# Performance work log

Measured on AMD Instinct MI355X. Metric: run time of the kernel, lower is better.

The kernel has to match this reference:

```python
import jax, jax.numpy as jnp
import numpy as np

N_NODES = 50000
N_EDGES = 150000
N_GRAPHS = 1024
IN_DIM = 78
OUT_DIM = 64
HEADS = 10
HID = OUT_DIM * HEADS  # 640
NEG_SLOPE = 0.2


def _add_self_loops(edge_index, num_nodes):
    loop = jnp.arange(num_nodes, dtype=edge_index.dtype)
    src = jnp.concatenate([edge_index[0], loop])
    dst = jnp.concatenate([edge_index[1], loop])
    return src, dst


def gatv2_conv(x, edge_index, Wl, Wr, att, bias, heads, out_dim):
    # PyG GATv2Conv (share_weights=False, concat=True, add_self_loops=True),
    # inference mode so attention dropout is a no-op.
    N = x.shape[0]
    src, dst = _add_self_loops(edge_index, N)
    xl = (x @ Wl).reshape(N, heads, out_dim)  # source transform
    xr = (x @ Wr).reshape(N, heads, out_dim)  # target transform
    s = jax.nn.leaky_relu(xl[src] + xr[dst], NEG_SLOPE)      # [E,H,C]
    logits = jnp.einsum('ehc,hc->eh', s, att)                # [E,H]
    m = jax.ops.segment_max(logits, dst, num_segments=N)     # [N,H] (self-loops => no empty segs)
    ex = jnp.exp(logits - m[dst])
    den = jax.ops.segment_sum(ex, dst, num_segments=N)
    alpha = ex / den[dst]                                    # scatter-softmax over in-edges
    out = jax.ops.segment_sum(alpha[:, :, None] * xl[src], dst, num_segments=N)
    return out.reshape(N, heads * out_dim) + bias


def gcn_conv(x, edge_index, W, b):
    N = x.shape[0]
    src, dst = _add_self_loops(edge_index, N)
    deg = jax.ops.segment_sum(jnp.ones(src.shape[0], x.dtype), dst, num_segments=N)
    dinv = jax.lax.rsqrt(jnp.maximum(deg, 1.0))
    norm = dinv[src] * dinv[dst]                             # [E]
    xw = x @ W
    return jax.ops.segment_sum(norm[:, None] * xw[src], dst, num_segments=N) + b


def setup_inputs() -> dict:
    key = jax.random.key(0)
    ks = jax.random.split(key, 16)
    x = jax.random.normal(ks[0], (N_NODES, IN_DIM), dtype=jnp.float32)
    edge_index = jax.random.randint(ks[1], (2, N_EDGES), 0, N_NODES, dtype=jnp.int64)
    batch = jnp.sort(jax.random.randint(ks[2], (N_NODES,), 0, N_GRAPHS, dtype=jnp.int64))

    def glorot(k, shape, fan_in):
        return jax.random.normal(k, shape, dtype=jnp.float32) * (1.0 / np.sqrt(fan_in))

    return {
        'x': x, 'edge_index': edge_index, 'batch': batch,
        'Wl1': glorot(ks[3], (IN_DIM, HID), IN_DIM),
        'Wr1': glorot(ks[4], (IN_DIM, HID), IN_DIM),
        'a1': glorot(ks[5], (HEADS, OUT_DIM), OUT_DIM),
        'b1': jnp.zeros((HID,), jnp.float32),
        'Wl2': glorot(ks[6], (HID, HID), HID),
        'Wr2': glorot(ks[7], (HID, HID), HID),
        'a2': glorot(ks[8], (1, HID), HID),
        'b2': jnp.zeros((HID,), jnp.float32),
        'Wg': glorot(ks[9], (HID, HID), HID),
        'bg': jnp.zeros((HID,), jnp.float32),
    }


def reference(x, edge_index, batch, Wl1, Wr1, a1, b1, Wl2, Wr2, a2, b2, Wg, bg):
    # inference: feature dropout layers are identity
    h = jax.nn.elu(gatv2_conv(x, edge_index, Wl1, Wr1, a1, b1, HEADS, OUT_DIM))
    h = gatv2_conv(h, edge_index, Wl2, Wr2, a2, b2, 1, HID)
    h = gcn_conv(h, edge_index, Wg, bg)
    h = jax.nn.relu(h)
    # global max pool + global mean pool per graph
    gmax = jax.ops.segment_max(h, batch, num_segments=N_GRAPHS)
    cnt = jax.ops.segment_sum(jnp.ones((h.shape[0],), h.dtype), batch, num_segments=N_GRAPHS)
    gmean = jax.ops.segment_sum(h, batch, num_segments=N_GRAPHS) / jnp.maximum(cnt, 1.0)[:, None]
    return jnp.concatenate([gmax, gmean], axis=1)
```

## Files before the change

### kernel.cpp

```cpp
#include <hip/hip_runtime.h>
#include <hip/hip_bf16.h>
#include <cstdint>
#include <cstddef>

typedef __hip_bfloat16 bf16;

#define N_NODES  50000
#define N_EDGES  150000
#define N_GRAPHS 1024
#define IN_DIM   78
#define K1P      128
#define OUT_DIM  64
#define HEADS    10
#define HID      640
#define NEG_SLOPE 0.2f
#define SCB      ((N_NODES + 255) / 256)

static __device__ __forceinline__ float b2f(bf16 v){ return __bfloat162float(v); }
static __device__ __forceinline__ bf16  f2b(float v){ return __float2bfloat16(v); }

__device__ __forceinline__ int clampi(int v, int hi){ return v < 0 ? 0 : (v >= hi ? hi - 1 : v); }

__device__ __forceinline__ float bf2f_bits(short s){
  return __uint_as_float(((unsigned)(unsigned short)s) << 16);
}
__device__ __forceinline__ short f2bf_bits(float v){
  unsigned u = __float_as_uint(v);
  return (short)((u + 0x7fffu + ((u >> 16) & 1u)) >> 16);
}

__global__ __launch_bounds__(256) void fill_u32(unsigned* __restrict__ p, unsigned v, int n){
  int i = blockIdx.x * 256 + threadIdx.x;
  if (i < n) p[i] = v;
}

__global__ __launch_bounds__(256) void conv_x(const float* __restrict__ x, bf16* __restrict__ XB){
  int i = blockIdx.x * 256 + threadIdx.x;
  if (i >= N_NODES * K1P) return;
  int n = i / K1P, k = i - n * K1P;
  XB[i] = f2b(k < IN_DIM ? x[(size_t)n * IN_DIM + k] : 0.f);
}

__global__ __launch_bounds__(256) void conv_wT2(const float* __restrict__ W0,
                                                const float* __restrict__ W1,
                                                bf16* __restrict__ WT,
                                                int K, int N, int Kp){
  int i = blockIdx.x * 256 + threadIdx.x;
  const int per = N * Kp;
  if (i >= 2 * per) return;
  int m = i / per, r = i - m * per;
  const float* W = m == 0 ? W0 : W1;
  int n = r / Kp, k = r - n * Kp;
  WT[i] = f2b(k < K ? W[(size_t)k * N + n] : 0.f);
}

__global__ __launch_bounds__(256) void conv_wT3t(const float* __restrict__ W0,
                                                 const float* __restrict__ W1,
                                                 const float* __restrict__ W2,
                                                 bf16* __restrict__ WT){
  __shared__ float t[32][33];
  int m = blockIdx.z;
  const float* W = m == 0 ? W0 : (m == 1 ? W1 : W2);
  int n0 = blockIdx.x * 32, k0 = blockIdx.y * 32;
  int tx = threadIdx.x & 31, ty = threadIdx.x >> 5;
#pragma unroll
  for (int r = 0; r < 32; r += 8)
    t[ty + r][tx] = W[(size_t)(k0 + ty + r) * HID + n0 + tx];
  __syncthreads();
  bf16* O = WT + (size_t)m * HID * HID;
#pragma unroll
  for (int r = 0; r < 32; r += 8)
    O[(size_t)(n0 + ty + r) * HID + k0 + tx] = f2b(t[tx][ty + r]);
}

#define BM 128
#define BN 128
#define BK 64

typedef __attribute__((ext_vector_type(8))) short bf16x8;
typedef __attribute__((ext_vector_type(4))) float f32x4;

typedef const __attribute__((address_space(1))) unsigned gu32;
typedef __attribute__((address_space(3))) unsigned lu32;

__global__ __launch_bounds__(256) void mfma_gemm(const bf16* __restrict__ A,
                                                 const bf16* __restrict__ BT,
                                                 bf16* __restrict__ C0,
                                                 bf16* __restrict__ C1,
                                                 int M, int Kp, int NB){
  int d   = blockIdx.x;
  int xcd = d & 7, j = d >> 3;
  int cb  = j % NB, ri = j / NB;
  int rb  = ri * 8 + xcd;
  const int row0 = rb * BM;
  if (row0 >= M) return;
  const int col0 = cb * BN;

  __shared__ short As[BM * BK];
  __shared__ short Bs[BN * BK];
  const int tid  = threadIdx.x;
  const int lane = tid & 63;
  const int wave = tid >> 6;
  const int wr   = (wave >> 1) * 64;
  const int wc   = (wave & 1) * 64;
  const int l15  = lane & 15;
  const int quad = lane >> 4;
  const int sw   = l15 & 7;

  const bf16* aptr[4];
  const bf16* bptr[4];
  lu32* lda[4];
  lu32* ldb[4];
#pragma unroll
  for (int t = 0; t < 4; ++t){
    int ci = (t * 4 + wave) * 64 + lane;
    int r  = ci >> 3;
    int sc = (ci & 7) ^ (r & 7);
    int gr = row0 + r; if (gr >= M) gr = M - 1;
    aptr[t] = A  + (size_t)gr * Kp + sc * 8;
    bptr[t] = BT + (size_t)(col0 + r) * Kp + sc * 8;
    lda[t]  = (lu32*)(&As[(t * 4 + wave) * 512]);
    ldb[t]  = (lu32*)(&Bs[(t * 4 + wave) * 512]);
  }

  f32x4 acc[4][4];
#pragma unroll
  for (int i = 0; i < 4; ++i)
#pragma unroll
    for (int jj = 0; jj < 4; ++jj) acc[i][jj] = (f32x4){0.f, 0.f, 0.f, 0.f};

  for (int k0 = 0; k0 < Kp; k0 += BK){
#pragma unroll
    for (int t = 0; t < 4; ++t){
      __builtin_amdgcn_global_load_lds((gu32*)(aptr[t] + k0), lda[t], 16, 0, 0);
      __builtin_amdgcn_global_load_lds((gu32*)(bptr[t] + k0), ldb[t], 16, 0, 0);
    }
    __syncthreads();

#pragma unroll
    for (int ks = 0; ks < 2; ++ks){
      const int slotA = ((ks * 4 + quad) ^ sw) * 8;
      bf16x8 af[4], bfr[4];
#pragma unroll
      for (int i = 0; i < 4; ++i)
        af[i] = *(bf16x8*)(&As[(wr + i * 16 + l15) * BK + slotA]);
#pragma unroll
      for (int jj = 0; jj < 4; ++jj)
        bfr[jj] = *(bf16x8*)(&Bs[(wc + jj * 16 + l15) * BK + slotA]);
#pragma unroll
      for (int i = 0; i < 4; ++i)
#pragma unroll
        for (int jj = 0; jj < 4; ++jj)
          acc[i][jj] = __builtin_amdgcn_mfma_f32_16x16x32_bf16(af[i], bfr[jj], acc[i][jj], 0, 0, 0);
    }
    __syncthreads();
  }

  if (row0 + BM <= M){
#pragma unroll
    for (int i = 0; i < 4; ++i){
#pragma unroll
      for (int jj = 0; jj < 4; ++jj){
        int gc = col0 + wc + jj * 16 + l15;
        bf16* Cp = (gc < HID) ? C0 : C1;
        size_t cc = (gc < HID) ? gc : gc - HID;
        size_t base = (size_t)(row0 + wr + i * 16 + quad * 4) * HID + cc;
#pragma unroll
        for (int r = 0; r < 4; ++r)
          Cp[base + (size_t)r * HID] = f2b(acc[i][jj][r]);
      }
    }
  } else {
#pragma unroll
    for (int i = 0; i < 4; ++i){
#pragma unroll
      for (int jj = 0; jj < 4; ++jj){
        int gc = col0 + wc + jj * 16 + l15;
        bf16* Cp = (gc < HID) ? C0 : C1;
        int cc   = (gc < HID) ? gc : gc - HID;
#pragma unroll
        for (int r = 0; r < 4; ++r){
          int gr = row0 + wr + i * 16 + quad * 4 + r;
          if (gr < M) Cp[(size_t)gr * HID + cc] = f2b(acc[i][jj][r]);
        }
      }
    }
  }
}

__global__ __launch_bounds__(256) void count_deg(const int* __restrict__ edst, int* __restrict__ degi){
  int e = blockIdx.x * 256 + threadIdx.x;
  if (e >= N_EDGES) return;
  atomicAdd(&degi[clampi(edst[e], N_NODES)], 1);
}

__global__ __launch_bounds__(256) void scan_blk(const int* __restrict__ degi,
                                                int* __restrict__ rowp,
                                                float* __restrict__ dinv,
                                                int* __restrict__ bsum){
  __shared__ int wsum[4];
  int b = blockIdx.x, tid = threadIdx.x;
  int i = b * 256 + tid;
  int lane = tid & 63, wv = tid >> 6;
  int v = (i < N_NODES) ? degi[i] : 0;
  int incl = v;
#pragma unroll
  for (int ofs = 1; ofs < 64; ofs <<= 1){
    int t = __shfl_up(incl, ofs);
    if (lane >= ofs) incl += t;
  }
  if (lane == 63) wsum[wv] = incl;
  __syncthreads();
  int woff = 0;
#pragma unroll
  for (int w = 0; w < 4; ++w) if (w < wv) woff += wsum[w];
  if (i < N_NODES){
    rowp[i] = woff + incl - v;
    dinv[i] = rsqrtf((float)(v + 1));
  }
  if (tid == 0) bsum[b] = wsum[0] + wsum[1] + wsum[2] + wsum[3];
}

__global__ __launch_bounds__(256) void scan_top(int* __restrict__ bsum, int* __restrict__ rowp){
  __shared__ int wsum[4];
  int tid = threadIdx.x, lane = tid & 63, wv = tid >> 6;
  int v = (tid < SCB) ? bsum[tid] : 0;
  int incl = v;
#pragma unroll
  for (int ofs = 1; ofs < 64; ofs <<= 1){
    int t = __shfl_up(incl, ofs);
    if (lane >= ofs) incl += t;
  }
  if (lane == 63) wsum[wv] = incl;
  __syncthreads();
  int woff = 0;
#pragma unroll
  for (int w = 0; w < 4; ++w) if (w < wv) woff += wsum[w];
  if (tid < SCB) bsum[tid] = woff + incl - v;
  if (tid == 255) rowp[N_NODES] = woff + incl;
}

__global__ __launch_bounds__(256) void scan_add(const int* __restrict__ bsum,
                                                int* __restrict__ rowp,
                                                int* __restrict__ curs){
  int i = blockIdx.x * 256 + threadIdx.x;
  if (i >= N_NODES) return;
  int r = rowp[i] + bsum[blockIdx.x];
  rowp[i] = r; curs[i] = r;
}

__global__ __launch_bounds__(256) void bucket_edges(const int* __restrict__ esrc,
                                                    const int* __restrict__ edst,
                                                    int* __restrict__ curs,
                                                    int* __restrict__ srcg,
                                                    int* __restrict__ dstg){
  int e = blockIdx.x * 256 + threadIdx.x;
  if (e >= N_EDGES) return;
  int d = clampi(edst[e], N_NODES);
  int pos = atomicAdd(&curs[d], 1);
  srcg[pos] = clampi(esrc[e], N_NODES);
  dstg[pos] = d;
}

__global__ __launch_bounds__(256) void gat1_fused(const bf16* __restrict__ xl,
                                                  const bf16* __restrict__ xr,
                                                  const int* __restrict__ srcg,
                                                  const int* __restrict__ rowp,
                                                  const float* __restrict__ att,
                                                  const float* __restrict__ bias,
                                                  bf16* __restrict__ H){
  int n    = (blockIdx.x * 256 + threadIdx.x) >> 6;
  int lane = threadIdx.x & 63;
  if (n >= N_NODES) return;
  int r0 = rowp[n], r1 = rowp[n + 1];

  float4 aA0 = *(const float4*)(att + 8 * lane);
  float4 aA1 = *(const float4*)(att + 8 * lane + 4);
  float2 aBv = *(const float2*)(att + 512 + 2 * lane);
  float attA[8] = {aA0.x, aA0.y, aA0.z, aA0.w, aA1.x, aA1.y, aA1.z, aA1.w};
  float attB0 = aBv.x, attB1 = aBv.y;

  const bf16* xrn = xr + (size_t)n * HID;
  bf16x8 vr = *(const bf16x8*)(xrn + 8 * lane);
  unsigned ur = *(const unsigned*)(xrn + 512 + 2 * lane);
  float xrA[8];
#pragma unroll
  for (int j = 0; j < 8; ++j) xrA[j] = bf2f_bits(vr[j]);
  float xrB0 = bf2f_bits((short)(ur & 0xffff));
  float xrB1 = bf2f_bits((short)(ur >> 16));

  auto logits = [&](const float* xA, float xB0, float xB1, float& lA, float& lB){
    float pa = 0.f;
#pragma unroll
    for (int j = 0; j < 8; ++j){
      float s = xA[j] + xrA[j];
      s *= (s > 0.f) ? 1.f : NEG_SLOPE;
      pa = fmaf(attA[j], s, pa);
    }
    pa += __shfl_xor(pa, 1);
    pa += __shfl_xor(pa, 2);
    pa += __shfl_xor(pa, 4);
    lA = pa;
    float s0 = xB0 + xrB0; s0 *= (s0 > 0.f) ? 1.f : NEG_SLOPE;
    float s1 = xB1 + xrB1; s1 *= (s1 > 0.f) ? 1.f : NEG_SLOPE;
    float pb = attB0 * s0 + attB1 * s1;
    pb += __shfl_xor(pb, 1);
    pb += __shfl_xor(pb, 2);
    pb += __shfl_xor(pb, 4);
    pb += __shfl_xor(pb, 8);
    pb += __shfl_xor(pb, 16);
    lB = pb;
  };

  float accA[8], accB0, accB1, lsA, lsB;
  float denA = 1.f, denB = 1.f;

  {
    const bf16* xn = xl + (size_t)n * HID;
    bf16x8 v0 = *(const bf16x8*)(xn + 8 * lane);
    unsigned u0 = *(const unsigned*)(xn + 512 + 2 * lane);
    float sA[8];
#pragma unroll
    for (int j = 0; j < 8; ++j){ sA[j] = bf2f_bits(v0[j]); accA[j] = sA[j]; }
    float sB0 = bf2f_bits((short)(u0 & 0xffff));
    float sB1 = bf2f_bits((short)(u0 >> 16));
    accB0 = sB0; accB1 = sB1;
    logits(sA, sB0, sB1, lsA, lsB);
  }

  auto upd1 = [&](const float* yA, float yB0, float yB1){
    float lA, lB;
    logits(yA, yB0, yB1, lA, lB);
    float pA = __expf(fminf(lA - lsA, 60.f));
    float pB = __expf(fminf(lB - lsB, 60.f));
    denA += pA; denB += pB;
#pragma unroll
    for (int j = 0; j < 8; ++j) accA[j] = fmaf(pA, yA[j], accA[j]);
    accB0 = fmaf(pB, yB0, accB0);
    accB1 = fmaf(pB, yB1, accB1);
  };

  int p = r0;
  for (; p + 3 < r1; p += 4){
    int s0i = srcg[p], s1i = srcg[p + 1], s2i = srcg[p + 2], s3i = srcg[p + 3];
    const bf16* q0 = xl + (size_t)s0i * HID;
    const bf16* q1 = xl + (size_t)s1i * HID;
    const bf16* q2 = xl + (size_t)s2i * HID;
    const bf16* q3 = xl + (size_t)s3i * HID;
    bf16x8 w0 = *(const bf16x8*)(q0 + 8 * lane);
    bf16x8 w1 = *(const bf16x8*)(q1 + 8 * lane);
    bf16x8 w2 = *(const bf16x8*)(q2 + 8 * lane);
    bf16x8 w3 = *(const bf16x8*)(q3 + 8 * lane);
    unsigned t0 = *(const unsigned*)(q0 + 512 + 2 * lane);
    unsigned t1 = *(const unsigned*)(q1 + 512 + 2 * lane);
    unsigned t2 = *(const unsigned*)(q2 + 512 + 2 * lane);
    unsigned t3 = *(const unsigned*)(q3 + 512 + 2 * lane);
    {
      float yA0[8];
#pragma unroll
      for (int j = 0; j < 8; ++j) yA0[j] = bf2f_bits(w0[j]);
      upd1(yA0, bf2f_bits((short)(t0 & 0xffff)), bf2f_bits((short)(t0 >> 16)));
    }
    {
      float yA1[8];
#pragma unroll
      for (int j = 0; j < 8; ++j) yA1[j] = bf2f_bits(w1[j]);
      upd1(yA1, bf2f_bits((short)(t1 & 0xffff)), bf2f_bits((short)(t1 >> 16)));
    }
    {
      float yA2[8];
#pragma unroll
      for (int j = 0; j < 8; ++j) yA2[j] = bf2f_bits(w2[j]);
      upd1(yA2, bf2f_bits((short)(t2 & 0xffff)), bf2f_bits((short)(t2 >> 16)));
    }
    {
      float yA3[8];
#pragma unroll
      for (int j = 0; j < 8; ++j) yA3[j] = bf2f_bits(w3[j]);
      upd1(yA3, bf2f_bits((short)(t3 & 0xffff)), bf2f_bits((short)(t3 >> 16)));
    }
  }
  for (; p < r1; ++p){
    int si = srcg[p];
    const bf16* q0 = xl + (size_t)si * HID;
    bf16x8 w0 = *(const bf16x8*)(q0 + 8 * lane);
    unsigned t0 = *(const unsigned*)(q0 + 512 + 2 * lane);
    float yA0[8];
#pragma unroll
    for (int j = 0; j < 8; ++j) yA0[j] = bf2f_bits(w0[j]);
    upd1(yA0, bf2f_bits((short)(t0 & 0xffff)), bf2f_bits((short)(t0 >> 16)));
  }

  float invA = 1.f / denA, invB = 1.f / denB;
  float4 bA0 = *(const float4*)(bias + 8 * lane);
  float4 bA1 = *(const float4*)(bias + 8 * lane + 4);
  float2 bB  = *(const float2*)(bias + 512 + 2 * lane);
  float bAa[8] = {bA0.x, bA0.y, bA0.z, bA0.w, bA1.x, bA1.y, bA1.z, bA1.w};
  bf16x8 oA;
#pragma unroll
  for (int j = 0; j < 8; ++j){
    float v = accA[j] * invA + bAa[j];
    v = v > 0.f ? v : (__expf(v) - 1.f);
    oA[j] = f2bf_bits(v);
  }
  float vb0 = accB0 * invB + bB.x; vb0 = vb0 > 0.f ? vb0 : (__expf(vb0) - 1.f);
  float vb1 = accB1 * invB + bB.y; vb1 = vb1 > 0.f ? vb1 : (__expf(vb1) - 1.f);
  bf16* hn = H + (size_t)n * HID;
  *(bf16x8*)(hn + 8 * lane) = oA;
  unsigned ob = (unsigned)(unsigned short)f2bf_bits(vb0) |
                ((unsigned)(unsigned short)f2bf_bits(vb1) << 16);
  *(unsigned*)(hn + 512 + 2 * lane) = ob;
}

__global__ __launch_bounds__(256) void gat2_fused(const bf16* __restrict__ xl,
                                                  const bf16* __restrict__ xr,
                                                  const int* __restrict__ srcg,
                                                  const int* __restrict__ rowp,
                                                  const float* __restrict__ att,
                                                  const float* __restrict__ bias,
                                                  bf16* __restrict__ H){
  int n    = (blockIdx.x * 256 + threadIdx.x) >> 6;
  int lane = threadIdx.x & 63;
  if (n >= N_NODES) return;
  int r0 = rowp[n], r1 = rowp[n + 1];

  float4 aA0 = *(const float4*)(att + 8 * lane);
  float4 aA1 = *(const float4*)(att + 8 * lane + 4);
  float2 aBv = *(const float2*)(att + 512 + 2 * lane);
  float attA[8] = {aA0.x, aA0.y, aA0.z, aA0.w, aA1.x, aA1.y, aA1.z, aA1.w};
  float attB0 = aBv.x, attB1 = aBv.y;

  const bf16* xrn = xr + (size_t)n * HID;
  bf16x8 vr = *(const bf16x8*)(xrn + 8 * lane);
  unsigned ur = *(const unsigned*)(xrn + 512 + 2 * lane);
  float xrA[8];
#pragma unroll
  for (int j = 0; j < 8; ++j) xrA[j] = bf2f_bits(vr[j]);
  float xrB0 = bf2f_bits((short)(ur & 0xffff));
  float xrB1 = bf2f_bits((short)(ur >> 16));

  auto logit1 = [&](const float* xA, float xB0, float xB1)->float{
    float s0 = xB0 + xrB0; s0 *= (s0 > 0.f) ? 1.f : NEG_SLOPE;
    float s1 = xB1 + xrB1; s1 *= (s1 > 0.f) ? 1.f : NEG_SLOPE;
    float pa = attB0 * s0 + attB1 * s1;
#pragma unroll
    for (int j = 0; j < 8; ++j){
      float s = xA[j] + xrA[j];
      s *= (s > 0.f) ? 1.f : NEG_SLOPE;
      pa = fmaf(attA[j], s, pa);
    }
    pa += __shfl_xor(pa, 1);
    pa += __shfl_xor(pa, 2);
    pa += __shfl_xor(pa, 4);
    pa += __shfl_xor(pa, 8);
    pa += __shfl_xor(pa, 16);
    pa += __shfl_xor(pa, 32);
    return pa;
  };

  float accA[8], accB0, accB1, ls;
  float den = 1.f;
  {
    const bf16* xn = xl + (size_t)n * HID;
    bf16x8 v0 = *(const bf16x8*)(xn + 8 * lane);
    unsigned u0 = *(const unsigned*)(xn + 512 + 2 * lane);
    float sA[8];
#pragma unroll
    for (int j = 0; j < 8; ++j){ sA[j] = bf2f_bits(v0[j]); accA[j] = sA[j]; }
    float sB0 = bf2f_bits((short)(u0 & 0xffff));
    float sB1 = bf2f_bits((short)(u0 >> 16));
    accB0 = sB0; accB1 = sB1;
    ls = logit1(sA, sB0, sB1);
  }

  auto upd1 = [&](const float* yA, float yB0, float yB1){
    float l = logit1(yA, yB0, yB1);
    float pv = __expf(fminf(l - ls, 60.f));
    den += pv;
#pragma unroll
    for (int j = 0; j < 8; ++j) accA[j] = fmaf(pv, yA[j], accA[j]);
    accB0 = fmaf(pv, yB0, accB0);
    accB1 = fmaf(pv, yB1, accB1);
  };

  int p = r0;
  for (; p + 3 < r1; p += 4){
    int s0i = srcg[p], s1i = srcg[p + 1], s2i = srcg[p + 2], s3i = srcg[p + 3];
    const bf16* q0 = xl + (size_t)s0i * HID;
    const bf16* q1 = xl + (size_t)s1i * HID;
    const bf16* q2 = xl + (size_t)s2i * HID;
    const bf16* q3 = xl + (size_t)s3i * HID;
    bf16x8 w0 = *(const bf16x8*)(q0 + 8 * lane);
    bf16x8 w1 = *(const bf16x8*)(q1 + 8 * lane);
    bf16x8 w2 = *(const bf16x8*)(q2 + 8 * lane);
    bf16x8 w3 = *(const bf16x8*)(q3 + 8 * lane);
    unsigned t0 = *(const unsigned*)(q0 + 512 + 2 * lane);
    unsigned t1 = *(const unsigned*)(q1 + 512 + 2 * lane);
    unsigned t2 = *(const unsigned*)(q2 + 512 + 2 * lane);
    unsigned t3 = *(const unsigned*)(q3 + 512 + 2 * lane);
    {
      float yA0[8];
#pragma unroll
      for (int j = 0; j < 8; ++j) yA0[j] = bf2f_bits(w0[j]);
      upd1(yA0, bf2f_bits((short)(t0 & 0xffff)), bf2f_bits((short)(t0 >> 16)));
    }
    {
      float yA1[8];
#pragma unroll
      for (int j = 0; j < 8; ++j) yA1[j] = bf2f_bits(w1[j]);
      upd1(yA1, bf2f_bits((short)(t1 & 0xffff)), bf2f_bits((short)(t1 >> 16)));
    }
    {
      float yA2[8];
#pragma unroll
      for (int j = 0; j < 8; ++j) yA2[j] = bf2f_bits(w2[j]);
      upd1(yA2, bf2f_bits((short)(t2 & 0xffff)), bf2f_bits((short)(t2 >> 16)));
    }
    {
      float yA3[8];
#pragma unroll
      for (int j = 0; j < 8; ++j) yA3[j] = bf2f_bits(w3[j]);
      upd1(yA3, bf2f_bits((short)(t3 & 0xffff)), bf2f_bits((short)(t3 >> 16)));
    }
  }
  for (; p < r1; ++p){
    int si = srcg[p];
    const bf16* q0 = xl + (size_t)si * HID;
    bf16x8 w0 = *(const bf16x8*)(q0 + 8 * lane);
    unsigned t0 = *(const unsigned*)(q0 + 512 + 2 * lane);
    float yA0[8];
#pragma unroll
    for (int j = 0; j < 8; ++j) yA0[j] = bf2f_bits(w0[j]);
    upd1(yA0, bf2f_bits((short)(t0 & 0xffff)), bf2f_bits((short)(t0 >> 16)));
  }

  float inv = 1.f / den;
  float4 bA0 = *(const float4*)(bias + 8 * lane);
  float4 bA1 = *(const float4*)(bias + 8 * lane + 4);
  float2 bB  = *(const float2*)(bias + 512 + 2 * lane);
  float bAa[8] = {bA0.x, bA0.y, bA0.z, bA0.w, bA1.x, bA1.y, bA1.z, bA1.w};
  bf16x8 oA;
#pragma unroll
  for (int j = 0; j < 8; ++j) oA[j] = f2bf_bits(accA[j] * inv + bAa[j]);
  bf16* hn = H + (size_t)n * HID;
  *(bf16x8*)(hn + 8 * lane) = oA;
  unsigned ob = (unsigned)(unsigned short)f2bf_bits(accB0 * inv + bB.x) |
                ((unsigned)(unsigned short)f2bf_bits(accB1 * inv + bB.y) << 16);
  *(unsigned*)(hn + 512 + 2 * lane) = ob;
}

__global__ __launch_bounds__(256) void gcn_gather(const bf16* __restrict__ xw,
                                                  const int* __restrict__ srcg,
                                                  const int* __restrict__ rowp,
                                                  const float* __restrict__ dinv,
                                                  const float* __restrict__ bg,
                                                  bf16* __restrict__ h3){
  int n    = (blockIdx.x * 256 + threadIdx.x) >> 6;
  int lane = threadIdx.x & 63;
  if (n >= N_NODES) return;
  int r0 = rowp[n], r1 = rowp[n + 1];

  float dn = dinv[n];
  float accA[8], accB[2];
  {
    float w = dn * dn;
    const bf16* xn = xw + (size_t)n * HID;
    bf16x8 va = *(const bf16x8*)(xn + 8 * lane);
    unsigned vb = *(const unsigned*)(xn + 512 + 2 * lane);
#pragma unroll
    for (int j = 0; j < 8; ++j) accA[j] = w * bf2f_bits(va[j]);
    accB[0] = w * bf2f_bits((short)(vb & 0xffff));
    accB[1] = w * bf2f_bits((short)(vb >> 16));
  }
  int p = r0;
  for (; p + 3 < r1; p += 4){
    int s0 = srcg[p], s1 = srcg[p + 1], s2 = srcg[p + 2], s3 = srcg[p + 3];
    const bf16* xs0 = xw + (size_t)s0 * HID;
    const bf16* xs1 = xw + (size_t)s1 * HID;
    const bf16* xs2 = xw + (size_t)s2 * HID;
    const bf16* xs3 = xw + (size_t)s3 * HID;
    float w0 = dinv[s0] * dn, w1 = dinv[s1] * dn, w2 = dinv[s2] * dn, w3 = dinv[s3] * dn;
    bf16x8 va0 = *(const bf16x8*)(xs0 + 8 * lane);
    bf16x8 va1 = *(const bf16x8*)(xs1 + 8 * lane);
    bf16x8 va2 = *(const bf16x8*)(xs2 + 8 * lane);
    bf16x8 va3 = *(const bf16x8*)(xs3 + 8 * lane);
    unsigned vb0 = *(const unsigned*)(xs0 + 512 + 2 * lane);
    unsigned vb1 = *(const unsigned*)(xs1 + 512 + 2 * lane);
    unsigned vb2 = *(const unsigned*)(xs2 + 512 + 2 * lane);
    unsigned vb3 = *(const unsigned*)(xs3 + 512 + 2 * lane);
#pragma unroll
    for (int j = 0; j < 8; ++j)
      accA[j] += w0 * bf2f_bits(va0[j]) + w1 * bf2f_bits(va1[j])
               + w2 * bf2f_bits(va2[j]) + w3 * bf2f_bits(va3[j]);
    accB[0] += w0 * bf2f_bits((short)(vb0 & 0xffff)) + w1 * bf2f_bits((short)(vb1 & 0xffff))
             + w2 * bf2f_bits((short)(vb2 & 0xffff)) + w3 * bf2f_bits((short)(vb3 & 0xffff));
    accB[1] += w0 * bf2f_bits((short)(vb0 >> 16))    + w1 * bf2f_bits((short)(vb1 >> 16))
             + w2 * bf2f_bits((short)(vb2 >> 16))    + w3 * bf2f_bits((short)(vb3 >> 16));
  }
  for (; p + 1 < r1; p += 2){
    int s0 = srcg[p], s1 = srcg[p + 1];
    float w0 = dinv[s0] * dn, w1 = dinv[s1] * dn;
    const bf16* xs0 = xw + (size_t)s0 * HID;
    const bf16* xs1 = xw + (size_t)s1 * HID;
    bf16x8 va0 = *(const bf16x8*)(xs0 + 8 * lane);
    bf16x8 va1 = *(const bf16x8*)(xs1 + 8 * lane);
    unsigned vb0 = *(const unsigned*)(xs0 + 512 + 2 * lane);
    unsigned vb1 = *(const unsigned*)(xs1 + 512 + 2 * lane);
#pragma unroll
    for (int j = 0; j < 8; ++j) accA[j] += w0 * bf2f_bits(va0[j]) + w1 * bf2f_bits(va1[j]);
    accB[0] += w0 * bf2f_bits((short)(vb0 & 0xffff)) + w1 * bf2f_bits((short)(vb1 & 0xffff));
    accB[1] += w0 * bf2f_bits((short)(vb0 >> 16))    + w1 * bf2f_bits((short)(vb1 >> 16));
  }
  if (p < r1){
    int s = srcg[p];
    float w = dinv[s] * dn;
    const bf16* xs = xw + (size_t)s * HID;
    bf16x8 va = *(const bf16x8*)(xs + 8 * lane);
    unsigned vb = *(const unsigned*)(xs + 512 + 2 * lane);
#pragma unroll
    for (int j = 0; j < 8; ++j) accA[j] += w * bf2f_bits(va[j]);
    accB[0] += w * bf2f_bits((short)(vb & 0xffff));
    accB[1] += w * bf2f_bits((short)(vb >> 16));
  }
  float4 bA0 = *(const float4*)(bg + 8 * lane);
  float4 bA1 = *(const float4*)(bg + 8 * lane + 4);
  float2 bB  = *(const float2*)(bg + 512 + 2 * lane);
  float bAa[8] = {bA0.x, bA0.y, bA0.z, bA0.w, bA1.x, bA1.y, bA1.z, bA1.w};
  bf16x8 oA;
#pragma unroll
  for (int j = 0; j < 8; ++j) oA[j] = f2bf_bits(fmaxf(accA[j] + bAa[j], 0.f));
  bf16* hn = h3 + (size_t)n * HID;
  *(bf16x8*)(hn + 8 * lane) = oA;
  unsigned ob = (unsigned)(unsigned short)f2bf_bits(fmaxf(accB[0] + bB.x, 0.f)) |
                ((unsigned)(unsigned short)f2bf_bits(fmaxf(accB[1] + bB.y, 0.f)) << 16);
  *(unsigned*)(hn + 512 + 2 * lane) = ob;
}

__global__ __launch_bounds__(256) void graph_bounds(const int* __restrict__ batch,
                                                    int* __restrict__ gstart){
  int n = blockIdx.x * 256 + threadIdx.x;
  if (n >= N_NODES) return;
  int b = clampi(batch[n], N_GRAPHS);
  if (n == 0){
    for (int g = 0; g <= b; ++g) gstart[g] = 0;
  } else {
    int bp = clampi(batch[n - 1], N_GRAPHS);
    for (int g = bp + 1; g <= b; ++g) gstart[g] = n;
  }
  if (n == N_NODES - 1){
    for (int g = b + 1; g <= N_GRAPHS; ++g) gstart[g] = N_NODES;
  }
}

__global__ __launch_bounds__(320) void pool_graph(const bf16* __restrict__ h3,
                                                  const int* __restrict__ gstart,
                                                  float* __restrict__ out){
  int g = blockIdx.x;
  int c2 = threadIdx.x;
  int n0 = gstart[g], n1 = gstart[g + 1];
  float mx0 = 0.f, mx1 = 0.f, sm0 = 0.f, sm1 = 0.f;
  for (int n = n0; n < n1; ++n){
    unsigned v = *(const unsigned*)(h3 + (size_t)n * HID + 2 * c2);
    float a = bf2f_bits((short)(v & 0xffff));
    float b = bf2f_bits((short)(v >> 16));
    mx0 = fmaxf(mx0, a); sm0 += a;
    mx1 = fmaxf(mx1, b); sm1 += b;
  }
  float inv = (n1 > n0) ? 1.f / (float)(n1 - n0) : 0.f;
  float* og = out + (size_t)g * 2 * HID;
  og[2 * c2]             = mx0;
  og[2 * c2 + 1]         = mx1;
  og[HID + 2 * c2]       = sm0 * inv;
  og[HID + 2 * c2 + 1]   = sm1 * inv;
}

extern "C" void kernel_launch(void* const* d_in, const int* in_sizes, int n_in,
                              void* d_out, int out_size, void* d_ws, size_t ws_size,
                              hipStream_t stream){
  const float* x     = (const float*)d_in[0];
  const int*   ei    = (const int*)d_in[1];
  const int*   batch = (const int*)d_in[2];
  const float* Wl1 = (const float*)d_in[3];
  const float* Wr1 = (const float*)d_in[4];
  const float* a1  = (const float*)d_in[5];
  const float* b1  = (const float*)d_in[6];
  const float* Wl2 = (const float*)d_in[7];
  const float* Wr2 = (const float*)d_in[8];
  const float* a2  = (const float*)d_in[9];
  const float* b2  = (const float*)d_in[10];
  const float* Wg  = (const float*)d_in[11];
  const float* bg  = (const float*)d_in[12];
  const int* esrc = ei;
  const int* edst = ei + N_EDGES;

  char* ws = (char*)d_ws;
  size_t off = 0;
  auto take = [&](size_t bytes)->char*{
    char* p = ws + off; off = (off + bytes + 255) & ~(size_t)255; return p;
  };
  bf16*     X1   = (bf16*)    take((size_t)N_NODES * HID * 2);
  bf16*     X2   = (bf16*)    take((size_t)N_NODES * HID * 2);
  bf16*     H    = (bf16*)    take((size_t)N_NODES * HID * 2);
  bf16*     XB   = (bf16*)    take((size_t)N_NODES * K1P * 2);
  bf16*     WT1l = (bf16*)    take((size_t)HID * K1P * 2);
  bf16*     WT1r = (bf16*)    take((size_t)HID * K1P * 2);
  bf16*     WT2l = (bf16*)    take((size_t)HID * HID * 2);
  bf16*     WT2r = (bf16*)    take((size_t)HID * HID * 2);
  bf16*     WTg  = (bf16*)    take((size_t)HID * HID * 2);
  int*      DEGI = (int*)     take((size_t)N_NODES * 4);
  int*      ROWP = (int*)     take((size_t)(N_NODES + 1) * 4);
  int*      CURS = (int*)     take((size_t)N_NODES * 4);
  int*      SRCG = (int*)     take((size_t)N_EDGES * 4);
  int*      DSTG = (int*)     take((size_t)N_EDGES * 4);
  float*    DINV = (float*)   take((size_t)N_NODES * 4);
  int*      GST  = (int*)     take((size_t)(N_GRAPHS + 1) * 4);
  int*      BSUM = (int*)     take((size_t)SCB * 4);
  (void)WT1r; (void)WT2r; (void)DSTG;

  dim3 blk(256);
  auto fill = [&](void* p, unsigned v, int n){
    fill_u32<<<dim3((n + 255) / 256), blk, 0, stream>>>((unsigned*)p, v, n);
  };
  const int MB8     = ((N_NODES + BM - 1) / BM + 7) / 8;
  const int nblocks = (N_NODES * 64 + 255) / 256;
  const int reblk   = (N_EDGES + 255) / 256;

  conv_x<<<(N_NODES * K1P + 255) / 256, blk, 0, stream>>>(x, XB);
  conv_wT2<<<(2 * HID * K1P + 255) / 256, blk, 0, stream>>>(Wl1, Wr1, WT1l, IN_DIM, HID, K1P);
  conv_wT3t<<<dim3(HID / 32, HID / 32, 3), blk, 0, stream>>>(Wl2, Wr2, Wg, WT2l);
  fill(DEGI, 0u, N_NODES);
  count_deg<<<reblk, blk, 0, stream>>>(edst, DEGI);
  scan_blk<<<dim3(SCB), blk, 0, stream>>>(DEGI, ROWP, DINV, BSUM);
  scan_top<<<dim3(1), blk, 0, stream>>>(BSUM, ROWP);
  scan_add<<<dim3(SCB), blk, 0, stream>>>(BSUM, ROWP, CURS);
  bucket_edges<<<reblk, blk, 0, stream>>>(esrc, edst, CURS, SRCG, DSTG);
  graph_bounds<<<(N_NODES + 255) / 256, blk, 0, stream>>>(batch, GST);

  mfma_gemm<<<dim3(8 * MB8 * 10), blk, 0, stream>>>(XB, WT1l, X1, X2, N_NODES, K1P, 10);
  gat1_fused<<<nblocks, blk, 0, stream>>>(X1, X2, SRCG, ROWP, a1, b1, H);

  mfma_gemm<<<dim3(8 * MB8 * 10), blk, 0, stream>>>(H, WT2l, X1, X2, N_NODES, HID, 10);
  gat2_fused<<<nblocks, blk, 0, stream>>>(X1, X2, SRCG, ROWP, a2, b2, H);

  mfma_gemm<<<dim3(8 * MB8 * 5), blk, 0, stream>>>(H, WTg, X1, X1, N_NODES, HID, 5);
  gcn_gather<<<nblocks, blk, 0, stream>>>(X1, SRCG, ROWP, DINV, bg, X2);
  pool_graph<<<dim3(N_GRAPHS), dim3(320), 0, stream>>>(X2, GST, (float*)d_out);
}
```

Baseline: 526.5 us.

## Fuse GCN neighbor gather with per-graph max/mean pooling

Replaces the separate GCN gather kernel and pooling kernel with a single per-graph kernel. Four waves each aggregate the nodes of a graph, apply bias and ReLU, and keep running max/sum in registers, then reduce through shared memory. This removes writing and re-reading the full node feature matrix and one launch. In exchange, parallelism drops to one block per graph, with serial per-wave node loops that can suffer if graph sizes are uneven.

Result: faster. 502.4 us, median of 2 (-4.6%).

```diff
diff --git a/kernel.cpp b/kernel.cpp
--- a/kernel.cpp
+++ b/kernel.cpp
@@ -549,91 +549,110 @@
   *(unsigned*)(hn + 512 + 2 * lane) = ob;
 }
 
-__global__ __launch_bounds__(256) void gcn_gather(const bf16* __restrict__ xw,
-                                                  const int* __restrict__ srcg,
-                                                  const int* __restrict__ rowp,
-                                                  const float* __restrict__ dinv,
-                                                  const float* __restrict__ bg,
-                                                  bf16* __restrict__ h3){
-  int n    = (blockIdx.x * 256 + threadIdx.x) >> 6;
+__global__ __launch_bounds__(256) void gcn_pool(const bf16* __restrict__ xw,
+                                                const int* __restrict__ srcg,
+                                                const int* __restrict__ rowp,
+                                                const float* __restrict__ dinv,
+                                                const float* __restrict__ bg,
+                                                const int* __restrict__ gstart,
+                                                float* __restrict__ out){
+  __shared__ float red[8][HID];
+  int g    = blockIdx.x;
+  int n0   = gstart[g], n1 = gstart[g + 1];
   int lane = threadIdx.x & 63;
-  if (n >= N_NODES) return;
-  int r0 = rowp[n], r1 = rowp[n + 1];
-
-  float dn = dinv[n];
-  float accA[8], accB[2];
-  {
-    float w = dn * dn;
-    const bf16* xn = xw + (size_t)n * HID;
-    bf16x8 va = *(const bf16x8*)(xn + 8 * lane);
-    unsigned vb = *(const unsigned*)(xn + 512 + 2 * lane);
-#pragma unroll
-    for (int j = 0; j < 8; ++j) accA[j] = w * bf2f_bits(va[j]);
-    accB[0] = w * bf2f_bits((short)(vb & 0xffff));
-    accB[1] = w * bf2f_bits((short)(vb >> 16));
-  }
-  int p = r0;
-  for (; p + 3 < r1; p += 4){
-    int s0 = srcg[p], s1 = srcg[p + 1], s2 = srcg[p + 2], s3 = srcg[p + 3];
-    const bf16* xs0 = xw + (size_t)s0 * HID;
-    const bf16* xs1 = xw + (size_t)s1 * HID;
-    const bf16* xs2 = xw + (size_t)s2 * HID;
-    const bf16* xs3 = xw + (size_t)s3 * HID;
-    float w0 = dinv[s0] * dn, w1 = dinv[s1] * dn, w2 = dinv[s2] * dn, w3 = dinv[s3] * dn;
-    bf16x8 va0 = *(const bf16x8*)(xs0 + 8 * lane);
-    bf16x8 va1 = *(const bf16x8*)(xs1 + 8 * lane);
-    bf16x8 va2 = *(const bf16x8*)(xs2 + 8 * lane);
-    bf16x8 va3 = *(const bf16x8*)(xs3 + 8 * lane);
-    unsigned vb0 = *(const unsigned*)(xs0 + 512 + 2 * lane);
-    unsigned vb1 = *(const unsigned*)(xs1 + 512 + 2 * lane);
-    unsigned vb2 = *(const unsigned*)(xs2 + 512 + 2 * lane);
-    unsigned vb3 = *(const unsigned*)(xs3 + 512 + 2 * lane);
-#pragma unroll
-    for (int j = 0; j < 8; ++j)
-      accA[j] += w0 * bf2f_bits(va0[j]) + w1 * bf2f_bits(va1[j])
-               + w2 * bf2f_bits(va2[j]) + w3 * bf2f_bits(va3[j]);
-    accB[0] += w0 * bf2f_bits((short)(vb0 & 0xffff)) + w1 * bf2f_bits((short)(vb1 & 0xffff))
-             + w2 * bf2f_bits((short)(vb2 & 0xffff)) + w3 * bf2f_bits((short)(vb3 & 0xffff));
-    accB[1] += w0 * bf2f_bits((short)(vb0 >> 16))    + w1 * bf2f_bits((short)(vb1 >> 16))
-             + w2 * bf2f_bits((short)(vb2 >> 16))    + w3 * bf2f_bits((short)(vb3 >> 16));
-  }
-  for (; p + 1 < r1; p += 2){
-    int s0 = srcg[p], s1 = srcg[p + 1];
-    float w0 = dinv[s0] * dn, w1 = dinv[s1] * dn;
-    const bf16* xs0 = xw + (size_t)s0 * HID;
-    const bf16* xs1 = xw + (size_t)s1 * HID;
-    bf16x8 va0 = *(const bf16x8*)(xs0 + 8 * lane);
-    bf16x8 va1 = *(const bf16x8*)(xs1 + 8 * lane);
-    unsigned vb0 = *(const unsigned*)(xs0 + 512 + 2 * lane);
-    unsigned vb1 = *(const unsigned*)(xs1 + 512 + 2 * lane);
-#pragma unroll
-    for (int j = 0; j < 8; ++j) accA[j] += w0 * bf2f_bits(va0[j]) + w1 * bf2f_bits(va1[j]);
-    accB[0] += w0 * bf2f_bits((short)(vb0 & 0xffff)) + w1 * bf2f_bits((short)(vb1 & 0xffff));
-    accB[1] += w0 * bf2f_bits((short)(vb0 >> 16))    + w1 * bf2f_bits((short)(vb1 >> 16));
-  }
-  if (p < r1){
-    int s = srcg[p];
-    float w = dinv[s] * dn;
-    const bf16* xs = xw + (size_t)s * HID;
-    bf16x8 va = *(const bf16x8*)(xs + 8 * lane);
-    unsigned vb = *(const unsigned*)(xs + 512 + 2 * lane);
-#pragma unroll
-    for (int j = 0; j < 8; ++j) accA[j] += w * bf2f_bits(va[j]);
-    accB[0] += w * bf2f_bits((short)(vb & 0xffff));
-    accB[1] += w * bf2f_bits((short)(vb >> 16));
-  }
+  int wv   = threadIdx.x >> 6;
+
   float4 bA0 = *(const float4*)(bg + 8 * lane);
   float4 bA1 = *(const float4*)(bg + 8 * lane + 4);
   float2 bB  = *(const float2*)(bg + 512 + 2 * lane);
   float bAa[8] = {bA0.x, bA0.y, bA0.z, bA0.w, bA1.x, bA1.y, bA1.z, bA1.w};
-  bf16x8 oA;
-#pragma unroll
-  for (int j = 0; j < 8; ++j) oA[j] = f2bf_bits(fmaxf(accA[j] + bAa[j], 0.f));
-  bf16* hn = h3 + (size_t)n * HID;
-  *(bf16x8*)(hn + 8 * lane) = oA;
-  unsigned ob = (unsigned)(unsigned short)f2bf_bits(fmaxf(accB[0] + bB.x, 0.f)) |
-                ((unsigned)(unsigned short)f2bf_bits(fmaxf(accB[1] + bB.y, 0.f)) << 16);
-  *(unsigned*)(hn + 512 + 2 * lane) = ob;
+
+  float mxA[8] = {0.f,0.f,0.f,0.f,0.f,0.f,0.f,0.f};
+  float smA[8] = {0.f,0.f,0.f,0.f,0.f,0.f,0.f,0.f};
+  float mxB0 = 0.f, mxB1 = 0.f, smB0 = 0.f, smB1 = 0.f;
+
+  for (int n = n0 + wv; n < n1; n += 4){
+    int r0 = rowp[n], r1 = rowp[n + 1];
+    float dn = dinv[n];
+    float accA[8], accB[2];
+    {
+      float w = dn * dn;
+      const bf16* xn = xw + (size_t)n * HID;
+      bf16x8 va = *(const bf16x8*)(xn + 8 * lane);
+      unsigned vb = *(const unsigned*)(xn + 512 + 2 * lane);
+#pragma unroll
+      for (int j = 0; j < 8; ++j) accA[j] = w * bf2f_bits(va[j]);
+      accB[0] = w * bf2f_bits((short)(vb & 0xffff));
+      accB[1] = w * bf2f_bits((short)(vb >> 16));
+    }
+    int p = r0;
+    for (; p + 3 < r1; p += 4){
+      int s0 = srcg[p], s1 = srcg[p + 1], s2 = srcg[p + 2], s3 = srcg[p + 3];
+      const bf16* xs0 = xw + (size_t)s0 * HID;
+      const bf16* xs1 = xw + (size_t)s1 * HID;
+      const bf16* xs2 = xw + (size_t)s2 * HID;
+      const bf16* xs3 = xw + (size_t)s3 * HID;
+      float w0 = dinv[s0] * dn, w1 = dinv[s1] * dn, w2 = dinv[s2] * dn, w3 = dinv[s3] * dn;
+      bf16x8 va0 = *(const bf16x8*)(xs0 + 8 * lane);
+      bf16x8 va1 = *(const bf16x8*)(xs1 + 8 * lane);
+      bf16x8 va2 = *(const bf16x8*)(xs2 + 8 * lane);
+      bf16x8 va3 = *(const bf16x8*)(xs3 + 8 * lane);
+      unsigned vb0 = *(const unsigned*)(xs0 + 512 + 2 * lane);
+      unsigned vb1 = *(const unsigned*)(xs1 + 512 + 2 * lane);
+      unsigned vb2 = *(const unsigned*)(xs2 + 512 + 2 * lane);
+      unsigned vb3 = *(const unsigned*)(xs3 + 512 + 2 * lane);
+#pragma unroll
+      for (int j = 0; j < 8; ++j)
+        accA[j] += w0 * bf2f_bits(va0[j]) + w1 * bf2f_bits(va1[j])
+                 + w2 * bf2f_bits(va2[j]) + w3 * bf2f_bits(va3[j]);
+      accB[0] += w0 * bf2f_bits((short)(vb0 & 0xffff)) + w1 * bf2f_bits((short)(vb1 & 0xffff))
+               + w2 * bf2f_bits((short)(vb2 & 0xffff)) + w3 * bf2f_bits((short)(vb3 & 0xffff));
+      accB[1] += w0 * bf2f_bits((short)(vb0 >> 16))    + w1 * bf2f_bits((short)(vb1 >> 16))
+               + w2 * bf2f_bits((short)(vb2 >> 16))    + w3 * bf2f_bits((short)(vb3 >> 16));
+    }
+    for (; p < r1; ++p){
+      int s = srcg[p];
+      float w = dinv[s] * dn;
+      const bf16* xs = xw + (size_t)s * HID;
+      bf16x8 va = *(const bf16x8*)(xs + 8 * lane);
+      unsigned vb = *(const unsigned*)(xs + 512 + 2 * lane);
+#pragma unroll
+      for (int j = 0; j < 8; ++j) accA[j] += w * bf2f_bits(va[j]);
+      accB[0] += w * bf2f_bits((short)(vb & 0xffff));
+      accB[1] += w * bf2f_bits((short)(vb >> 16));
+    }
+#pragma unroll
+    for (int j = 0; j < 8; ++j){
+      float v = fmaxf(accA[j] + bAa[j], 0.f);
+      mxA[j] = fmaxf(mxA[j], v); smA[j] += v;
+    }
+    {
+      float v0 = fmaxf(accB[0] + bB.x, 0.f);
+      float v1 = fmaxf(accB[1] + bB.y, 0.f);
+      mxB0 = fmaxf(mxB0, v0); smB0 += v0;
+      mxB1 = fmaxf(mxB1, v1); smB1 += v1;
+    }
+  }
+
+#pragma unroll
+  for (int j = 0; j < 8; ++j){
+    red[wv][8 * lane + j]     = mxA[j];
+    red[4 + wv][8 * lane + j] = smA[j];
+  }
+  red[wv][512 + 2 * lane]         = mxB0;
+  red[wv][512 + 2 * lane + 1]     = mxB1;
+  red[4 + wv][512 + 2 * lane]     = smB0;
+  red[4 + wv][512 + 2 * lane + 1] = smB1;
+  __syncthreads();
+
+  float inv = (n1 > n0) ? 1.f / (float)(n1 - n0) : 0.f;
+  float* og = out + (size_t)g * 2 * HID;
+  for (int c = threadIdx.x; c < HID; c += 256){
+    float mx = fmaxf(fmaxf(red[0][c], red[1][c]), fmaxf(red[2][c], red[3][c]));
+    float sm = red[4][c] + red[5][c] + red[6][c] + red[7][c];
+    og[c]       = mx;
+    og[HID + c] = sm * inv;
+  }
 }
 
 __global__ __launch_bounds__(256) void graph_bounds(const int* __restrict__ batch,
@@ -650,28 +669,6 @@
   if (n == N_NODES - 1){
     for (int g = b + 1; g <= N_GRAPHS; ++g) gstart[g] = N_NODES;
   }
-}
-
-__global__ __launch_bounds__(320) void pool_graph(const bf16* __restrict__ h3,
-                                                  const int* __restrict__ gstart,
-                                                  float* __restrict__ out){
-  int g = blockIdx.x;
-  int c2 = threadIdx.x;
-  int n0 = gstart[g], n1 = gstart[g + 1];
-  float mx0 = 0.f, mx1 = 0.f, sm0 = 0.f, sm1 = 0.f;
-  for (int n = n0; n < n1; ++n){
-    unsigned v = *(const unsigned*)(h3 + (size_t)n * HID + 2 * c2);
-    float a = bf2f_bits((short)(v & 0xffff));
-    float b = bf2f_bits((short)(v >> 16));
-    mx0 = fmaxf(mx0, a); sm0 += a;
-    mx1 = fmaxf(mx1, b); sm1 += b;
-  }
-  float inv = (n1 > n0) ? 1.f / (float)(n1 - n0) : 0.f;
-  float* og = out + (size_t)g * 2 * HID;
-  og[2 * c2]             = mx0;
-  og[2 * c2 + 1]         = mx1;
-  og[HID + 2 * c2]       = sm0 * inv;
-  og[HID + 2 * c2 + 1]   = sm1 * inv;
 }
 
 extern "C" void kernel_launch(void* const* d_in, const int* in_sizes, int n_in,
@@ -715,7 +712,7 @@
   float*    DINV = (float*)   take((size_t)N_NODES * 4);
   int*      GST  = (int*)     take((size_t)(N_GRAPHS + 1) * 4);
   int*      BSUM = (int*)     take((size_t)SCB * 4);
-  (void)WT1r; (void)WT2r; (void)DSTG;
+  (void)WT1r; (void)WT2r; (void)DSTG; (void)X2;
 
   dim3 blk(256);
   auto fill = [&](void* p, unsigned v, int n){
@@ -743,6 +740,5 @@
   gat2_fused<<<nblocks, blk, 0, stream>>>(X1, X2, SRCG, ROWP, a2, b2, H);
 
   mfma_gemm<<<dim3(8 * MB8 * 5), blk, 0, stream>>>(H, WTg, X1, X1, N_NODES, HID, 5);
-  gcn_gather<<<nblocks, blk, 0, stream>>>(X1, SRCG, ROWP, DINV, bg, X2);
-  pool_graph<<<dim3(N_GRAPHS), dim3(320), 0, stream>>>(X2, GST, (float*)d_out);
-}
+  gcn_pool<<<dim3(N_GRAPHS), blk, 0, stream>>>(X1, SRCG, ROWP, DINV, bg, GST, (float*)d_out);
+}
```
